# Kernel optimization log

Hardware: AMD Instinct MI355X
Metric: run time of the kernel (lower is better)

Reference implementation:

```python
import jax, jax.numpy as jnp
import numpy as np
from jax import lax

WIN = 11
NUM_CLASSES = 2
WEIGHTS = (1.0, 0.5)
PAD = (WIN - 1) // 2


def _edge_kernel():
    w = -jnp.ones((1, 1, WIN, WIN), jnp.float32)
    return w.at[0, 0, WIN // 2, WIN // 2].set(WIN * WIN - 1.0)


def setup_inputs() -> dict:
    key = jax.random.key(0)
    k0, k1, k2 = jax.random.split(key, 3)
    B, H, W = 16, 1024, 1024
    score0 = jax.random.normal(k0, (B, NUM_CLASSES, H, W), jnp.float32)
    score1 = jax.random.normal(k1, (B, NUM_CLASSES, H, W), jnp.float32)
    target = jax.random.randint(k2, (B, 1, H, W), 0, NUM_CLASSES, jnp.int32)
    return {"score0": score0, "score1": score1, "target": target}


def _loss_one(x, onehot, edge_mask, smoothing):
    # x: [B,C,H,W] logits; onehot: [B,C,H,W]; edge_mask: [B,1,H,W]
    log_p = jax.nn.log_softmax(x, axis=1)
    alpha = smoothing
    # softlabel: filled with alpha, target class gets 1 - alpha + alpha/C
    soft = alpha + onehot * (1.0 - 2.0 * alpha + alpha / NUM_CLASSES)
    mask = onehot * (1.0 - edge_mask) + soft * edge_mask
    # sum over class dim, mean over (B,H,W), negated
    return -jnp.mean(jnp.sum(mask * log_p, axis=1))


def reference(score0, score1, target):
    tgt_f = target.astype(jnp.float32)  # [B,1,H,W]
    edge = lax.conv_general_dilated(
        tgt_f, _edge_kernel(), window_strides=(1, 1),
        padding=((PAD, PAD), (PAD, PAD)),
        dimension_numbers=("NCHW", "OIHW", "NCHW"))
    edge_mask = (edge != 0).astype(jnp.float32)          # [B,1,H,W]
    smoothing = jnp.minimum(jnp.mean(edge_mask), 0.2)
    cls = jnp.arange(NUM_CLASSES, dtype=jnp.int32).reshape(1, NUM_CLASSES, 1, 1)
    onehot = (target == cls).astype(jnp.float32)         # [B,C,H,W]
    loss = (WEIGHTS[0] * _loss_one(score0, onehot, edge_mask, smoothing)
            + WEIGHTS[1] * _loss_one(score1, onehot, edge_mask, smoothing))
    return loss
```

## Files before the change

kernel.cpp:

```cpp
#include <hip/hip_runtime.h>

typedef float v2f __attribute__((ext_vector_type(2)));
typedef unsigned long long u64;

#define NPIX 16777216.0

#define TBITS_OFF 0u
#define EBITS_OFF (2u*1024u*1024u)
#define PART_OFF  (4u*1024u*1024u)
#define NB5       2048

#define TW   128
#define TH   32
#define HALO 5
#define TIW  (TW + 2*HALO)
#define TIH  (TH + 2*HALO)
#define TB_P 144
#define VS_P 142
#define NBX  8
#define NBY  32
#define NBZ  16
#define NB   (NBX*NBY*NBZ)

__device__ __forceinline__ unsigned nib(int4 r) {
    return (unsigned)((r.x & 1) | ((r.y & 1) << 1) | ((r.z & 1) << 2) | ((r.w & 1) << 3));
}

__global__ __launch_bounds__(256)
void pack_bits32(const int* __restrict__ target, unsigned int* __restrict__ tb32) {
    const int G = blockIdx.x * 256 + threadIdx.x;
    const int4* p = (const int4*)target + (size_t)G * 8;
    const int4 r0 = p[0], r1 = p[1], r2 = p[2], r3 = p[3];
    const int4 r4 = p[4], r5 = p[5], r6 = p[6], r7 = p[7];
    unsigned m = nib(r0);
    m |= nib(r1) << 4;
    m |= nib(r2) << 8;
    m |= nib(r3) << 12;
    m |= nib(r4) << 16;
    m |= nib(r5) << 20;
    m |= nib(r6) << 24;
    m |= nib(r7) << 28;
    tb32[G] = m;
}

__device__ __forceinline__ u64 hor11_or(u64 L, u64 M, u64 R) {
    u64 o = M;
    o |= (M >> 1) | (R << 63);
    o |= (M >> 2) | (R << 62);
    o |= (M >> 3) | (R << 61);
    o |= (M >> 4) | (R << 60);
    o |= (M >> 5) | (R << 59);
    o |= (M << 1) | (L >> 63);
    o |= (M << 2) | (L >> 62);
    o |= (M << 3) | (L >> 61);
    o |= (M << 4) | (L >> 60);
    o |= (M << 5) | (L >> 59);
    return o;
}
__device__ __forceinline__ u64 hor11_and(u64 L, u64 M, u64 R) {
    u64 a = M;
    a &= (M >> 1) | (R << 63);
    a &= (M >> 2) | (R << 62);
    a &= (M >> 3) | (R << 61);
    a &= (M >> 4) | (R << 60);
    a &= (M >> 5) | (R << 59);
    a &= (M << 1) | (L >> 63);
    a &= (M << 2) | (L >> 62);
    a &= (M << 3) | (L >> 61);
    a &= (M << 4) | (L >> 60);
    a &= (M << 5) | (L >> 59);
    return a;
}

__global__ __launch_bounds__(256)
void edge_bits(const u64* __restrict__ tbits, u64* __restrict__ ebits) {
    const int idx = blockIdx.x * 256 + threadIdx.x;
    const int wi  = idx & 15;
    const int row = (idx >> 4) & 1023;
    const int b   = idx >> 14;
    const u64* plane = tbits + (size_t)b * 16384;

    u64 oL = 0, oM = 0, oR = 0;
    u64 aL = ~0ull, aM = ~0ull, aR = ~0ull;
    #pragma unroll
    for (int dr = -5; dr <= 5; ++dr) {
        const int r = row + dr;
        u64 L = 0, M = 0, R = 0;
        if ((unsigned)r < 1024u) {
            const u64* rp = plane + (size_t)r * 16;
            L = (wi > 0)  ? rp[wi - 1] : 0ull;
            M = rp[wi];
            R = (wi < 15) ? rp[wi + 1] : 0ull;
        }
        oL |= L; oM |= M; oR |= R;
        aL &= L; aM &= M; aR &= R;
    }
    const u64 O = hor11_or(oL, oM, oR);
    const u64 A = hor11_and(aL, aM, aR);
    ebits[idx] = O ^ A;
}

__device__ __forceinline__ void acc_pair(v2f p0, v2f p1, unsigned t0, unsigned t1,
                                         v2f ef, v2f& s1, v2f& s2) {
    v2f d = p0 - p1;
    v2f sp;
    sp.x = __logf(1.0f + __expf(-fabsf(d.x)));
    sp.y = __logf(1.0f + __expf(-fabsf(d.y)));
    v2f m;
    m.x = fmaxf(p0.x, p1.x);
    m.y = fmaxf(p0.y, p1.y);
    v2f lse = m + sp;
    v2f pt;
    pt.x = t0 ? p1.x : p0.x;
    pt.y = t1 ? p1.y : p0.y;
    v2f lpt = pt - lse;
    v2f slp = (p0 + p1) - 2.0f * lse;
    s1 += lpt;
    s2 += ef * (slp - 1.5f * lpt);
}

__device__ __forceinline__ void proc_group(float4 x0, float4 x1, float4 y0, float4 y1,
                                           unsigned nt, unsigned ne,
                                           v2f& cntv, v2f& a1, v2f& a2, v2f& b1, v2f& b2) {
    #pragma unroll
    for (int h = 0; h < 2; ++h) {
        const unsigned t0 = (nt >> (2 * h)) & 1u;
        const unsigned t1 = (nt >> (2 * h + 1)) & 1u;
        const unsigned e0 = (ne >> (2 * h)) & 1u;
        const unsigned e1 = (ne >> (2 * h + 1)) & 1u;
        v2f ef; ef.x = (float)e0; ef.y = (float)e1;
        cntv += ef;
        v2f p0, p1, q0, q1;
        p0.x = h ? x0.z : x0.x;  p0.y = h ? x0.w : x0.y;
        p1.x = h ? x1.z : x1.x;  p1.y = h ? x1.w : x1.y;
        q0.x = h ? y0.z : y0.x;  q0.y = h ? y0.w : y0.y;
        q1.x = h ? y1.z : y1.x;  q1.y = h ? y1.w : y1.y;
        acc_pair(p0, p1, t0, t1, ef, a1, a2);
        acc_pair(q0, q1, t0, t1, ef, b1, b2);
    }
}

#define DECLB(B) float4 x0##B, x1##B, y0##B, y1##B; unsigned tw##B, ew##B;
#define LOADI(B, k) \
    x0##B = *(const float4*)(p0 + (k) * 1024u); \
    x1##B = *(const float4*)(p0 + 1048576u + (k) * 1024u); \
    y0##B = *(const float4*)(p1 + (k) * 1024u); \
    y1##B = *(const float4*)(p1 + 1048576u + (k) * 1024u); \
    tw##B = tb32[wbase + (k) * 32u]; \
    ew##B = eb32[wbase + (k) * 32u];
#define COMPI(B) { \
    const unsigned nt = (tw##B >> shift) & 15u; \
    const unsigned ne = (ew##B >> shift) & 15u; \
    proc_group(x0##B, x1##B, y0##B, y1##B, nt, ne, cntv, a1, a2, b1, b2); }

__global__ __launch_bounds__(256)
void loss_stream5(const float* __restrict__ score0,
                  const float* __restrict__ score1,
                  const unsigned int* __restrict__ tb32,
                  const unsigned int* __restrict__ eb32,
                  float* __restrict__ partials) {
    __shared__ float red[4][5];
    const int tid = threadIdx.x;
    const int bid = blockIdx.x;

    const int      bb    = bid >> 7;
    const unsigned r0    = ((unsigned)bid & 127u) * 8192u + 4u * (unsigned)tid;
    const unsigned wbase = ((unsigned)bid * 8192u + 4u * (unsigned)tid) >> 5;
    const unsigned shift = (4u * (unsigned)tid) & 31u;

    const float* p0 = score0 + (size_t)bb * 2097152u + r0;
    const float* p1 = score1 + (size_t)bb * 2097152u + r0;

    DECLB(A) DECLB(B) DECLB(C)

    v2f cntv = {0.f, 0.f}, a1 = {0.f, 0.f}, a2 = {0.f, 0.f};
    v2f b1 = {0.f, 0.f}, b2 = {0.f, 0.f};

    LOADI(A, 0) LOADI(B, 1)
    COMPI(A)    LOADI(C, 2)
    COMPI(B)    LOADI(A, 3)
    COMPI(C)    LOADI(B, 4)
    COMPI(A)    LOADI(C, 5)
    COMPI(B)    LOADI(A, 6)
    COMPI(C)    LOADI(B, 7)
    COMPI(A)
    COMPI(B)

    float vals[5] = {cntv.x + cntv.y, a1.x + a1.y, a2.x + a2.y,
                     b1.x + b1.y, b2.x + b2.y};
    const int lane = tid & 63, wv = tid >> 6;
    #pragma unroll
    for (int q = 0; q < 5; ++q) {
        float v = vals[q];
        #pragma unroll
        for (int off = 32; off > 0; off >>= 1) v += __shfl_down(v, off);
        if (lane == 0) red[wv][q] = v;
    }
    __syncthreads();
    if (tid == 0) {
        #pragma unroll
        for (int q = 0; q < 5; ++q)
            partials[q * NB5 + bid] = red[0][q] + red[1][q] + red[2][q] + red[3][q];
    }
}

__global__ __launch_bounds__(1024)
void finalize_loss(const float* __restrict__ ws, float* __restrict__ out, int n) {
    __shared__ double red[16][5];
    const int tid = threadIdx.x;
    double acc[5] = {0, 0, 0, 0, 0};
    for (int i = tid; i < n; i += 1024) {
        #pragma unroll
        for (int q = 0; q < 5; ++q) acc[q] += (double)ws[q * n + i];
    }
    const int lane = tid & 63, wv = tid >> 6;
    #pragma unroll
    for (int q = 0; q < 5; ++q) {
        double v = acc[q];
        #pragma unroll
        for (int off = 32; off > 0; off >>= 1) v += __shfl_down(v, off);
        if (lane == 0) red[wv][q] = v;
    }
    __syncthreads();
    if (tid == 0) {
        double s[5];
        #pragma unroll
        for (int q = 0; q < 5; ++q) {
            double v = 0;
            for (int w = 0; w < 16; ++w) v += red[w][q];
            s[q] = v;
        }
        const double N = NPIX;
        double alpha = s[0] / N;
        if (alpha > 0.2) alpha = 0.2;
        double loss = (s[1] + alpha * s[2]) + 0.5 * (s[3] + alpha * s[4]);
        out[0] = (float)(-loss / N);
    }
}

__global__ __launch_bounds__(256)
void fused_edge_loss(const float* __restrict__ score0,
                     const float* __restrict__ score1,
                     const int*   __restrict__ target,
                     float*       __restrict__ ws) {
    __shared__ unsigned char  tb[TIH][TB_P];
    __shared__ unsigned short vs[TH][VS_P];
    __shared__ float          red[4][5];

    const int tid   = threadIdx.x;
    const int tileX = blockIdx.x * TW;
    const int tileY = blockIdx.y * TH;
    const int b     = blockIdx.z;
    const int bid   = (blockIdx.z * NBY + blockIdx.y) * NBX + blockIdx.x;

    const int* tgt = target + (size_t)b * (1024 * 1024);

    for (int idx = tid; idx < TIH * TIW; idx += 256) {
        int rr = idx / TIW;
        int cc = idx - rr * TIW;
        int gr = tileY + rr - HALO;
        int gc = tileX + cc - HALO;
        unsigned char v = 0;
        if ((unsigned)gr < 1024u && (unsigned)gc < 1024u)
            v = (unsigned char)tgt[gr * 1024 + gc];
        tb[rr][cc] = v;
    }
    __syncthreads();

    if (tid < TIW) {
        int acc = 0;
        #pragma unroll
        for (int rr = 0; rr < 11; ++rr) acc += tb[rr][tid];
        vs[0][tid] = (unsigned short)acc;
        for (int r = 1; r < TH; ++r) {
            acc += (int)tb[r + 10][tid] - (int)tb[r - 1][tid];
            vs[r][tid] = (unsigned short)acc;
        }
    }
    __syncthreads();

    const float* s0b = score0 + (size_t)b * (2 * 1024 * 1024);
    const float* s1b = score1 + (size_t)b * (2 * 1024 * 1024);
    const int tx = tid & 31;
    const int ty = tid >> 5;

    float cnt = 0.f, a1 = 0.f, a2 = 0.f, b1 = 0.f, b2 = 0.f;

    #pragma unroll
    for (int p = 0; p < 4; ++p) {
        const int r  = ty + p * 8;
        const int gr = tileY + r;
        const int c0 = tx * 4;
        const int gc = tileX + c0;

        int S[4];
        int s = 0;
        #pragma unroll
        for (int k = 0; k < 11; ++k) s += vs[r][c0 + k];
        S[0] = s;
        #pragma unroll
        for (int j = 1; j < 4; ++j) {
            s += (int)vs[r][c0 + 10 + j] - (int)vs[r][c0 + j - 1];
            S[j] = s;
        }

        const size_t base = (size_t)gr * 1024 + gc;
        float4 x0 = *(const float4*)(s0b + base);
        float4 x1 = *(const float4*)(s0b + 1048576 + base);
        float4 y0 = *(const float4*)(s1b + base);
        float4 y1 = *(const float4*)(s1b + 1048576 + base);
        float p0a[4] = {x0.x, x0.y, x0.z, x0.w};
        float p1a[4] = {x1.x, x1.y, x1.z, x1.w};
        float q0a[4] = {y0.x, y0.y, y0.z, y0.w};
        float q1a[4] = {y1.x, y1.y, y1.z, y1.w};

        #pragma unroll
        for (int j = 0; j < 4; ++j) {
            const int t = tb[r + 5][c0 + 5 + j];
            const float e = (S[j] != 121 * t) ? 1.0f : 0.0f;
            cnt += e;
            {
                float p0 = p0a[j], p1 = p1a[j];
                float m   = fmaxf(p0, p1);
                float lse = m + __logf(1.0f + __expf(-fabsf(p0 - p1)));
                float lpt = (t ? p1 : p0) - lse;
                float slp = p0 + p1 - 2.0f * lse;
                a1 += lpt;
                a2 += e * (slp - 1.5f * lpt);
            }
            {
                float q0 = q0a[j], q1 = q1a[j];
                float m   = fmaxf(q0, q1);
                float lse = m + __logf(1.0f + __expf(-fabsf(q0 - q1)));
                float lpt = (t ? q1 : q0) - lse;
                float slp = q0 + q1 - 2.0f * lse;
                b1 += lpt;
                b2 += e * (slp - 1.5f * lpt);
            }
        }
    }

    float vals[5] = {cnt, a1, a2, b1, b2};
    const int lane = tid & 63, wv = tid >> 6;
    #pragma unroll
    for (int q = 0; q < 5; ++q) {
        float v = vals[q];
        #pragma unroll
        for (int off = 32; off > 0; off >>= 1) v += __shfl_down(v, off);
        if (lane == 0) red[wv][q] = v;
    }
    __syncthreads();
    if (tid == 0) {
        #pragma unroll
        for (int q = 0; q < 5; ++q) {
            float v = red[0][q] + red[1][q] + red[2][q] + red[3][q];
            ws[q * NB + bid] = v;
        }
    }
}

extern "C" void kernel_launch(void* const* d_in, const int* in_sizes, int n_in,
                              void* d_out, int out_size, void* d_ws, size_t ws_size,
                              hipStream_t stream) {
    const float* score0 = (const float*)d_in[0];
    const float* score1 = (const float*)d_in[1];
    const int*   target = (const int*)d_in[2];
    float* out = (float*)d_out;
    unsigned char* ws = (unsigned char*)d_ws;

    const size_t need = (size_t)PART_OFF + (size_t)5 * NB5 * 4;
    if (ws_size >= need) {
        unsigned int* tb = (unsigned int*)(ws + TBITS_OFF);
        u64*          eb = (u64*)(ws + EBITS_OFF);
        float*  partials = (float*)(ws + PART_OFF);
        pack_bits32<<<2048, 256, 0, stream>>>(target, tb);
        edge_bits<<<1024, 256, 0, stream>>>((const u64*)tb, eb);
        loss_stream5<<<NB5, 256, 0, stream>>>(score0, score1,
                                              (const unsigned int*)tb,
                                              (const unsigned int*)eb, partials);
        finalize_loss<<<1, 1024, 0, stream>>>(partials, out, NB5);
    } else {
        float* partials = (float*)ws;
        dim3 grid(NBX, NBY, NBZ);
        fused_edge_loss<<<grid, 256, 0, stream>>>(score0, score1, target, partials);
        finalize_loss<<<1, 1024, 0, stream>>>(partials, out, NB);
    }
}
```

Baseline: 324.0 us.

## Stream logits through LDS via async global_load_lds with double buffering

The streaming loss kernel now has each wave load one plane (score0/score1, class 0/1) straight into shared memory using global_load_lds, with two buffers and explicit vmcnt waits and barriers. All threads then read their float4 groups back from LDS for the computation. The mask words are hoisted and loaded up front. The aim is to cut register pressure and issue overhead on the dominant HBM stream so more bytes stay in flight. The cost is barrier synchronisation and extra LDS traffic, and the hand-written waitcnt must stay correct.

After: 331.6 us. 2.3% more time.

```diff
diff --git a/kernel.cpp b/kernel.cpp
--- a/kernel.cpp
+++ b/kernel.cpp
@@ -8,7 +8,7 @@
 #define TBITS_OFF 0u
 #define EBITS_OFF (2u*1024u*1024u)
 #define PART_OFF  (4u*1024u*1024u)
-#define NB5       2048
+#define NB6       2048
 
 #define TW   128
 #define TH   32
@@ -140,67 +140,88 @@
     }
 }
 
-#define DECLB(B) float4 x0##B, x1##B, y0##B, y1##B; unsigned tw##B, ew##B;
-#define LOADI(B, k) \
-    x0##B = *(const float4*)(p0 + (k) * 1024u); \
-    x1##B = *(const float4*)(p0 + 1048576u + (k) * 1024u); \
-    y0##B = *(const float4*)(p1 + (k) * 1024u); \
-    y1##B = *(const float4*)(p1 + 1048576u + (k) * 1024u); \
-    tw##B = tb32[wbase + (k) * 32u]; \
-    ew##B = eb32[wbase + (k) * 32u];
-#define COMPI(B) { \
-    const unsigned nt = (tw##B >> shift) & 15u; \
-    const unsigned ne = (ew##B >> shift) & 15u; \
-    proc_group(x0##B, x1##B, y0##B, y1##B, nt, ne, cntv, a1, a2, b1, b2); }
+__device__ __forceinline__ void gload16(const float* g, float* l) {
+    __builtin_amdgcn_global_load_lds(
+        (const __attribute__((address_space(1))) void*)g,
+        (__attribute__((address_space(3))) void*)l,
+        16, 0, 0);
+}
+
+#define WAITV4 asm volatile("s_waitcnt vmcnt(4)" ::: "memory")
+#define WAITV0 asm volatile("s_waitcnt vmcnt(0)" ::: "memory")
+#define BAR    __builtin_amdgcn_s_barrier()
+#define SCHED0 __builtin_amdgcn_sched_barrier(0)
+
+#define STAGE6(k, b) \
+    gload16(plane + (k) * 1024u +   0u + 4u * lane, &lds[b][w][  0]); \
+    gload16(plane + (k) * 1024u + 256u + 4u * lane, &lds[b][w][256]); \
+    gload16(plane + (k) * 1024u + 512u + 4u * lane, &lds[b][w][512]); \
+    gload16(plane + (k) * 1024u + 768u + 4u * lane, &lds[b][w][768]);
+
+#define MASKL(k) const unsigned tw##k = tb32[gw0 + (k) * 32u], \
+                                ew##k = eb32[gw0 + (k) * 32u];
+
+#define COMPT6(k, b) { \
+    const float4 X0 = *(const float4*)&lds[b][0][tid4]; \
+    const float4 X1 = *(const float4*)&lds[b][1][tid4]; \
+    const float4 Y0 = *(const float4*)&lds[b][2][tid4]; \
+    const float4 Y1 = *(const float4*)&lds[b][3][tid4]; \
+    proc_group(X0, X1, Y0, Y1, (tw##k >> shift) & 15u, (ew##k >> shift) & 15u, \
+               cntv, a1, a2, b1, b2); }
 
 __global__ __launch_bounds__(256)
-void loss_stream5(const float* __restrict__ score0,
+void loss_stream6(const float* __restrict__ score0,
                   const float* __restrict__ score1,
                   const unsigned int* __restrict__ tb32,
                   const unsigned int* __restrict__ eb32,
                   float* __restrict__ partials) {
+    __shared__ float lds[2][4][1024];
     __shared__ float red[4][5];
     const int tid = threadIdx.x;
     const int bid = blockIdx.x;
-
-    const int      bb    = bid >> 7;
-    const unsigned r0    = ((unsigned)bid & 127u) * 8192u + 4u * (unsigned)tid;
-    const unsigned wbase = ((unsigned)bid * 8192u + 4u * (unsigned)tid) >> 5;
+    const int w   = tid >> 6;
+    const unsigned lane = (unsigned)(tid & 63);
+
+    const int      bb  = bid >> 7;
+    const unsigned inb = ((unsigned)bid & 127u) * 8192u;
+
+    const float* plane = ((w & 2) ? score1 : score0)
+                       + (size_t)bb * 2097152u + (unsigned)(w & 1) * 1048576u + inb;
+
+    const unsigned gw0   = ((unsigned)bb * 1048576u + inb + 4u * (unsigned)tid) >> 5;
     const unsigned shift = (4u * (unsigned)tid) & 31u;
-
-    const float* p0 = score0 + (size_t)bb * 2097152u + r0;
-    const float* p1 = score1 + (size_t)bb * 2097152u + r0;
-
-    DECLB(A) DECLB(B) DECLB(C)
+    MASKL(0) MASKL(1) MASKL(2) MASKL(3) MASKL(4) MASKL(5) MASKL(6) MASKL(7)
+
+    const unsigned tid4 = 4u * (unsigned)tid;
 
     v2f cntv = {0.f, 0.f}, a1 = {0.f, 0.f}, a2 = {0.f, 0.f};
     v2f b1 = {0.f, 0.f}, b2 = {0.f, 0.f};
 
-    LOADI(A, 0) LOADI(B, 1)
-    COMPI(A)    LOADI(C, 2)
-    COMPI(B)    LOADI(A, 3)
-    COMPI(C)    LOADI(B, 4)
-    COMPI(A)    LOADI(C, 5)
-    COMPI(B)    LOADI(A, 6)
-    COMPI(C)    LOADI(B, 7)
-    COMPI(A)
-    COMPI(B)
+    STAGE6(0, 0) STAGE6(1, 1)
+    WAITV4; BAR; SCHED0; COMPT6(0, 0); SCHED0; BAR; STAGE6(2, 0)
+    WAITV4; BAR; SCHED0; COMPT6(1, 1); SCHED0; BAR; STAGE6(3, 1)
+    WAITV4; BAR; SCHED0; COMPT6(2, 0); SCHED0; BAR; STAGE6(4, 0)
+    WAITV4; BAR; SCHED0; COMPT6(3, 1); SCHED0; BAR; STAGE6(5, 1)
+    WAITV4; BAR; SCHED0; COMPT6(4, 0); SCHED0; BAR; STAGE6(6, 0)
+    WAITV4; BAR; SCHED0; COMPT6(5, 1); SCHED0; BAR; STAGE6(7, 1)
+    WAITV4; BAR; SCHED0; COMPT6(6, 0); SCHED0;
+    WAITV0; BAR; SCHED0; COMPT6(7, 1);
 
     float vals[5] = {cntv.x + cntv.y, a1.x + a1.y, a2.x + a2.y,
                      b1.x + b1.y, b2.x + b2.y};
-    const int lane = tid & 63, wv = tid >> 6;
+    const int lane_ = tid & 63, wv = tid >> 6;
     #pragma unroll
     for (int q = 0; q < 5; ++q) {
         float v = vals[q];
         #pragma unroll
         for (int off = 32; off > 0; off >>= 1) v += __shfl_down(v, off);
-        if (lane == 0) red[wv][q] = v;
+        if (lane_ == 0) red[wv][q] = v;
     }
     __syncthreads();
     if (tid == 0) {
         #pragma unroll
         for (int q = 0; q < 5; ++q)
-            partials[q * NB5 + bid] = red[0][q] + red[1][q] + red[2][q] + red[3][q];
+            partials[q * NB6 + bid] = red[0][q] + red[1][q] + red[2][q] + red[3][q];
     }
 }
 
@@ -368,17 +389,17 @@
     float* out = (float*)d_out;
     unsigned char* ws = (unsigned char*)d_ws;
 
-    const size_t need = (size_t)PART_OFF + (size_t)5 * NB5 * 4;
+    const size_t need = (size_t)PART_OFF + (size_t)5 * NB6 * 4;
     if (ws_size >= need) {
         unsigned int* tb = (unsigned int*)(ws + TBITS_OFF);
         u64*          eb = (u64*)(ws + EBITS_OFF);
         float*  partials = (float*)(ws + PART_OFF);
         pack_bits32<<<2048, 256, 0, stream>>>(target, tb);
         edge_bits<<<1024, 256, 0, stream>>>((const u64*)tb, eb);
-        loss_stream5<<<NB5, 256, 0, stream>>>(score0, score1,
+        loss_stream6<<<NB6, 256, 0, stream>>>(score0, score1,
                                               (const unsigned int*)tb,
                                               (const unsigned int*)eb, partials);
-        finalize_loss<<<1, 1024, 0, stream>>>(partials, out, NB5);
+        finalize_loss<<<1, 1024, 0, stream>>>(partials, out, NB6);
     } else {
         float* partials = (float*)ws;
         dim3 grid(NBX, NBY, NBZ);
```
